# Performance work log

Hardware: AMD Instinct MI355X
Metric: run time of the kernel (lower is better)

Reference implementation:

```python
import jax, jax.numpy as jnp
import numpy as np

CHANNEL = 512
NUM_HEAD = 8
HEAD_DIM = CHANNEL // NUM_HEAD  # 64
TEMP = (2.0 * HEAD_DIM) ** 0.5  # sqrt(temperature_coeff * d)
B, N = 4, 2048


def setup_inputs() -> dict:
    key = jax.random.key(0)
    kx, km, kq, kk, kv = jax.random.split(key, 5)
    scale = 1.0 / np.sqrt(CHANNEL)
    return {
        "x": jax.random.normal(kx, (B, N, CHANNEL), dtype=jnp.float32),
        "mask": jax.random.randint(km, (1, B, N, N), 0, 2).astype(bool),
        "Wq": jax.random.normal(kq, (CHANNEL, CHANNEL), dtype=jnp.float32) * scale,
        "Wk": jax.random.normal(kk, (CHANNEL, CHANNEL), dtype=jnp.float32) * scale,
        "Wv": jax.random.normal(kv, (CHANNEL, CHANNEL), dtype=jnp.float32) * scale,
    }


def reference(x, mask, Wq, Wk, Wv):
    b, n, f = x.shape
    # nn.Linear(bias=False): y = x @ W.T ; split into heads
    q = (x @ Wq.T).reshape(b, n, NUM_HEAD, HEAD_DIM)
    k = (x @ Wk.T).reshape(b, n, NUM_HEAD, HEAD_DIM)
    v = (x @ Wv.T).reshape(b, n, NUM_HEAD, HEAD_DIM)
    # scores laid out as (head, batch, q, k) to match torch permute(2,0,1,3)
    a = jnp.einsum("bqhd,bkhd->hbqk", q, k) / TEMP
    # mask (1,B,N,N) broadcasts over the head dim; True -> -inf (masked_fill)
    alpha = jax.nn.softmax(jnp.where(mask, -jnp.inf, a), axis=-1)
    # (alpha @ v) then permute back to (b, n, h, d) and merge heads
    out = jnp.einsum("hbqk,bkhd->bqhd", alpha, v).reshape(b, n, f)
    return out
```

## Files before the change

kernel.cpp:

```cpp
#include <hip/hip_runtime.h>


typedef float f32x4 __attribute__((ext_vector_type(4)));
typedef float f32x16 __attribute__((ext_vector_type(16)));
typedef short short8 __attribute__((ext_vector_type(8)));

#define MFMA16(a, b, c) __builtin_amdgcn_mfma_f32_16x16x32_bf16((a), (b), (c), 0, 0, 0)
#define MFMA32(a, b, c) __builtin_amdgcn_mfma_f32_32x32x16_bf16((a), (b), (c), 0, 0, 0)

#if __has_builtin(__builtin_amdgcn_exp2f)
#define EXP2(x) __builtin_amdgcn_exp2f(x)
#else
#define EXP2(x) exp2f(x)
#endif

#define NBH 32
#define NSEQ 2048
#define DH 64

__device__ __forceinline__ unsigned short f2bf(float f) {
  unsigned int u = __float_as_uint(f);
  u += 0x7fffu + ((u >> 16) & 1u);
  return (unsigned short)(u >> 16);
}
__device__ __forceinline__ float bf2f(unsigned short h) {
  return __uint_as_float(((unsigned int)h) << 16);
}
__device__ __forceinline__ void split_bf16(float f, unsigned short& hi, unsigned short& lo) {
  hi = f2bf(f);
  lo = f2bf(f - bf2f(hi));
}

__device__ __forceinline__ unsigned cvtpk_bf16(float a, float b) {
  unsigned d;
  asm("v_cvt_pk_bf16_f32 %0, %1, %2" : "=v"(d) : "v"(a), "v"(b));
  return d;
}
__device__ __forceinline__ void permswap(unsigned& a, unsigned& b) {
  asm("v_permlane32_swap_b32 %0, %1" : "+v"(a), "+v"(b));
}
template <bool S2>
__device__ __forceinline__ void xsw(unsigned ce, unsigned co, unsigned& lo, unsigned& hi) {
  if (S2) { permswap(ce, co); }
  else    { permswap(co, ce); }
  lo = ce;
  hi = co;
}

typedef __attribute__((address_space(1))) const unsigned int as1_u32;
typedef __attribute__((address_space(3))) unsigned int as3_u32;
__device__ __forceinline__ void gld_lds16(const unsigned short* g, unsigned short* l) {
  __builtin_amdgcn_global_load_lds((as1_u32*)g, (as3_u32*)l, 16, 0, 0);
}

__global__ __launch_bounds__(256) void prep_kernel(
    const void* __restrict__ mraw, unsigned long long* __restrict__ Mp,
    const float* __restrict__ x,
    const float* __restrict__ Wq, const float* __restrict__ Wk, const float* __restrict__ Wv,
    unsigned short* __restrict__ xh, unsigned short* __restrict__ xl,
    unsigned short* __restrict__ wh, unsigned short* __restrict__ wl) {
  const int tid = threadIdx.x;
  __shared__ int s_bad;
  if (tid == 0) s_bad = 0;
  __syncthreads();
  const unsigned int* mw32 = (const unsigned int*)mraw;
  {
    unsigned int w0 = mw32[tid], w1 = mw32[256 + tid];
    bool ok = (w0 == 0u || w0 == 1u || w0 == 0x3f800000u) &&
              (w1 == 0u || w1 == 1u || w1 == 0x3f800000u);
    if (!ok) s_bad = 1;
  }
  __syncthreads();
  const size_t e0 = (size_t)blockIdx.x * 16384 + (size_t)tid * 64;
  unsigned long long bits = 0ull;
  if (s_bad == 0) {
    const uint4* p = (const uint4*)mw32 + (e0 >> 2);
#pragma unroll
    for (int j = 0; j < 16; ++j) {
      uint4 v = p[j];
      unsigned nib = (v.x != 0u) | ((v.y != 0u) << 1) | ((v.z != 0u) << 2) | ((v.w != 0u) << 3);
      bits |= (unsigned long long)nib << (j * 4);
    }
  } else {
    const uint4* p = (const uint4*)((const unsigned char*)mraw + e0);
#pragma unroll
    for (int j = 0; j < 4; ++j) {
      uint4 v = p[j];
      unsigned dw[4] = {v.x, v.y, v.z, v.w};
#pragma unroll
      for (int d = 0; d < 4; ++d) {
        unsigned nib = (((dw[d]) & 0xffu) != 0u) | ((((dw[d] >> 8) & 0xffu) != 0u) << 1) |
                       ((((dw[d] >> 16) & 0xffu) != 0u) << 2) | ((((dw[d] >> 24) & 0xffu) != 0u) << 3);
        bits |= (unsigned long long)nib << ((j * 4 + d) * 4);
      }
    }
  }
  Mp[e0 >> 6] = bits;

  const int gtid = blockIdx.x * 256 + tid;
  const float4* x4 = (const float4*)x;
#pragma unroll
  for (int rep = 0; rep < 4; ++rep) {
    int i = gtid + rep * 262144;
    float4 v = x4[i];
    unsigned short h0, l0, h1, l1, h2, l2, h3, l3;
    split_bf16(v.x, h0, l0); split_bf16(v.y, h1, l1);
    split_bf16(v.z, h2, l2); split_bf16(v.w, h3, l3);
    *(ushort4*)&xh[(size_t)i * 4] = make_ushort4(h0, h1, h2, h3);
    *(ushort4*)&xl[(size_t)i * 4] = make_ushort4(l0, l1, l2, l3);
  }
  if (gtid < 65536) {
    const float* Ws[3] = {Wq, Wk, Wv};
#pragma unroll
    for (int z = 0; z < 3; ++z) {
      float4 v = ((const float4*)Ws[z])[gtid];
      unsigned short h0, l0, h1, l1, h2, l2, h3, l3;
      split_bf16(v.x, h0, l0); split_bf16(v.y, h1, l1);
      split_bf16(v.z, h2, l2); split_bf16(v.w, h3, l3);
      size_t o = (size_t)z * 262144 + (size_t)gtid * 4;
      *(ushort4*)&wh[o] = make_ushort4(h0, h1, h2, h3);
      *(ushort4*)&wl[o] = make_ushort4(l0, l1, l2, l3);
    }
  }
}

__global__ __launch_bounds__(256, 4) void proj_kernel(
    const unsigned short* __restrict__ xh, const unsigned short* __restrict__ xl,
    const unsigned short* __restrict__ wh, const unsigned short* __restrict__ wl,
    unsigned short* __restrict__ Qh, unsigned short* __restrict__ Kh,
    unsigned short* __restrict__ Vh) {
  const int tid = threadIdx.x;
  const int w = tid >> 6, l = tid & 63;
  const int m0 = blockIdx.x * 64;
  const int h = blockIdx.y;
  const int lrow = l & 15, lg = l >> 4;
  const int rw = (w >> 1) * 32, cw = (w & 1) * 32;

  union LDSU {
    unsigned short tiles[8][64][32];
    unsigned short ob[64][72];
  };
  __shared__ __align__(16) LDSU u;

  f32x4 acc[3][2][2] = {};

  const unsigned short* planes[8] = {xh, xl, wh, wl, wh + 262144, wl + 262144,
                                     wh + 524288, wl + 524288};
  const int rowb[8] = {m0, m0, h * 64, h * 64, h * 64, h * 64, h * 64, h * 64};
  const int srow = l >> 2, scol = (l & 3) * 8;
  const unsigned short* s0 = planes[2 * w] + (size_t)(rowb[2 * w] + srow) * 512 + scol;
  const unsigned short* s1 = planes[2 * w + 1] + (size_t)(rowb[2 * w + 1] + srow) * 512 + scol;
  unsigned short* d0 = &u.tiles[2 * w][0][0];
  unsigned short* d1 = &u.tiles[2 * w + 1][0][0];

  for (int k0 = 0; k0 < 512; k0 += 32) {
    __syncthreads();
#pragma unroll
    for (int c = 0; c < 4; ++c) {
      gld_lds16(s0 + k0 + c * 8192, d0 + c * 512);
      gld_lds16(s1 + k0 + c * 8192, d1 + c * 512);
    }
    __syncthreads();

    short8 axh[2], axl[2];
#pragma unroll
    for (int t = 0; t < 2; ++t) {
      axh[t] = *(const short8*)&u.tiles[0][rw + 16 * t + lrow][lg * 8];
      axl[t] = *(const short8*)&u.tiles[1][rw + 16 * t + lrow][lg * 8];
    }
#pragma unroll
    for (int z = 0; z < 3; ++z) {
      short8 bh[2], bl[2];
#pragma unroll
      for (int t = 0; t < 2; ++t) {
        bh[t] = *(const short8*)&u.tiles[2 + 2 * z][cw + 16 * t + lrow][lg * 8];
        bl[t] = *(const short8*)&u.tiles[3 + 2 * z][cw + 16 * t + lrow][lg * 8];
      }
#pragma unroll
      for (int tm = 0; tm < 2; ++tm)
#pragma unroll
        for (int tn = 0; tn < 2; ++tn) {
          acc[z][tm][tn] = MFMA16(axh[tm], bh[tn], acc[z][tm][tn]);
          acc[z][tm][tn] = MFMA16(axh[tm], bl[tn], acc[z][tm][tn]);
          acc[z][tm][tn] = MFMA16(axl[tm], bh[tn], acc[z][tm][tn]);
        }
    }
  }

  const float qsc = 1.4426950408889634f * 0.08838834764831845f;
  const int orow = tid >> 2, oc = (tid & 3) * 16;
  const int b = m0 >> 11, n0 = m0 & 2047, bhid = b * 8 + h;
#pragma unroll
  for (int z = 0; z < 3; ++z) {
    __syncthreads();
#pragma unroll
    for (int tm = 0; tm < 2; ++tm)
#pragma unroll
      for (int tn = 0; tn < 2; ++tn) {
        int dcol = cw + tn * 16 + lrow;
        int nl = rw + tm * 16 + lg * 4;
#pragma unroll
        for (int r = 0; r < 4; ++r) {
          float v = acc[z][tm][tn][r];
          if (z == 0) v *= qsc;
          if (z < 2) u.ob[nl + r][dcol] = f2bf(v);
          else       u.ob[dcol][nl + r] = f2bf(v);
        }
      }
    __syncthreads();
    if (z < 2) {
      unsigned short* O = (z == 0) ? Qh : Kh;
      size_t base = ((size_t)bhid * 2048 + n0 + orow) * 64 + oc;
      *(short8*)&O[base] = *(const short8*)&u.ob[orow][oc];
      *(short8*)&O[base + 8] = *(const short8*)&u.ob[orow][oc + 8];
    } else {
      size_t vb = ((size_t)bhid * 64 + orow) * 2048 + n0 + oc;
      *(short8*)&Vh[vb] = *(const short8*)&u.ob[orow][oc];
      *(short8*)&Vh[vb + 8] = *(const short8*)&u.ob[orow][oc + 8];
    }
  }
}

template <bool S2>
__device__ __forceinline__ void attn_body(
    unsigned short (&kvb)[2][4][64][64],
    const unsigned short* __restrict__ Qh,
    const unsigned short* __restrict__ Kh, const unsigned short* __restrict__ Vh,
    const unsigned long long* __restrict__ Mp, float* __restrict__ out) {
  const int tid = threadIdx.x;
  const int w = tid >> 6, l = tid & 63;
  const int wl = blockIdx.x;
  const int rm = (wl & 7) * 64 + (wl >> 3);
  const int q0 = (rm & 15) * 128;
  const int bh = rm >> 4;
  const int b = bh >> 3, h = bh & 7;
  const int l31 = l & 31, hi = l >> 5;
  const int swz = (l31 & 7) << 4;

  const unsigned short* Qhb = Qh + (size_t)bh * NSEQ * DH;
  const unsigned short* Khb = Kh + (size_t)bh * NSEQ * DH;
  const unsigned short* Vhb = Vh + (size_t)bh * DH * NSEQ;
  const unsigned long long* Mb = Mp + (size_t)b * NSEQ * 32;
  float* Ob = out + (size_t)b * NSEQ * 512 + h * 64;

  char* kv0 = (char*)&kvb[0][0][0][0];

  int va[4];
#pragma unroll
  for (int d = 0; d < 4; ++d) va[d] = l31 * 128 + (((d * 32) | (hi * 16)) ^ swz);

  const size_t qoff = (size_t)(q0 + w * 32 + l31) * 64 + hi * 8;
  short8 qh[4];
#pragma unroll
  for (int d = 0; d < 4; ++d) qh[d] = *(const short8*)(Qhb + qoff + d * 16);

  short8 ones;
#pragma unroll
  for (int j = 0; j < 8; ++j) ones[j] = (short)0x3F80;

  f32x16 o[2] = {};
  f32x16 osum = {};
  float mrun = -1e30f;
  const int qglob = q0 + w * 32 + l31;

  const int row0 = tid >> 3, colx = (tid & 7) * 8;
  const int swst = (colx * 2) ^ ((row0 & 7) << 4);
  int dstK[4], dstV[4];
#pragma unroll
  for (int c = 0; c < 4; ++c) {
    const int rsub = (c & 1) * 32 + row0;
    dstK[c] = (c >> 1) * 8192 + rsub * 128 + swst;
    dstV[c] = 16384 + (c >> 1) * 8192 + rsub * 128 + swst;
  }
  size_t koff[4], voff[4];
#pragma unroll
  for (int c = 0; c < 4; ++c) {
    koff[c] = (size_t)(c * 32 + row0) * 64 + colx;
    voff[c] = (size_t)((c & 1) * 32 + row0) * 2048 + (c >> 1) * 64 + colx;
  }

  short8 sk[4], sv[4];
#pragma unroll
  for (int c = 0; c < 4; ++c) {
    sk[c] = *(const short8*)(Khb + koff[c]);
    sv[c] = *(const short8*)(Vhb + voff[c]);
  }
#pragma unroll
  for (int c = 0; c < 4; ++c) {
    *(short8*)(kv0 + dstK[c]) = sk[c];
    *(short8*)(kv0 + dstV[c]) = sv[c];
  }
#pragma unroll
  for (int c = 0; c < 4; ++c) {
    koff[c] += 8192; voff[c] += 128;
    sk[c] = *(const short8*)(Khb + koff[c]);
    sv[c] = *(const short8*)(Vhb + voff[c]);
  }
  __syncthreads();

  for (int it = 0; it < 16; ++it) {
    char* cur = kv0 + (size_t)(it & 1) * 32768;
    if (it < 15) {
      char* nb = kv0 + (size_t)((it + 1) & 1) * 32768;
#pragma unroll
      for (int c = 0; c < 4; ++c) {
        *(short8*)(nb + dstK[c]) = sk[c];
        *(short8*)(nb + dstV[c]) = sv[c];
      }
      if (it < 14) {
#pragma unroll
        for (int c = 0; c < 4; ++c) {
          koff[c] += 8192; voff[c] += 128;
          sk[c] = *(const short8*)(Khb + koff[c]);
          sv[c] = *(const short8*)(Vhb + voff[c]);
        }
      }
    }

    f32x16 sA[2] = {}, sB[2] = {};
    __builtin_amdgcn_s_setprio(1);
#pragma unroll
    for (int d = 0; d < 4; ++d) {
#pragma unroll
      for (int kt = 0; kt < 2; ++kt) {
        short8 kfa = *(const short8*)(cur + kt * 4096 + va[d]);
        short8 kfb = *(const short8*)(cur + 8192 + kt * 4096 + va[d]);
        sA[kt] = MFMA32(kfa, qh[d], sA[kt]);
        sB[kt] = MFMA32(kfb, qh[d], sB[kt]);
      }
    }
    __builtin_amdgcn_s_setprio(0);

    const unsigned long long mwA = Mb[(size_t)qglob * 32 + 2 * it];
    const unsigned long long mwB = Mb[(size_t)qglob * 32 + 2 * it + 1];
#pragma unroll
    for (int kt = 0; kt < 2; ++kt)
#pragma unroll
      for (int m = 0; m < 4; ++m) {
        unsigned nibA = ((unsigned)(mwA >> (kt * 32 + m * 8 + 4 * hi))) & 0xFu;
        unsigned nibB = ((unsigned)(mwB >> (kt * 32 + m * 8 + 4 * hi))) & 0xFu;
#pragma unroll
        for (int r = 0; r < 4; ++r) {
          sA[kt][4 * m + r] = ((nibA >> r) & 1u) ? -1e30f : sA[kt][4 * m + r];
          sB[kt][4 * m + r] = ((nibB >> r) & 1u) ? -1e30f : sB[kt][4 * m + r];
        }
      }

    float mx = fmaxf(sA[0][0], sB[0][0]);
#pragma unroll
    for (int kt = 0; kt < 2; ++kt)
#pragma unroll
      for (int e = (kt == 0 ? 1 : 0); e < 16; ++e)
        mx = fmaxf(fmaxf(sA[kt][e], sB[kt][e]), mx);
    mx = fmaxf(mx, __shfl_xor(mx, 32));
    const bool grow = __any(mx > mrun + 11.0f);
    const float mnew = grow ? fmaxf(mrun, mx) : mrun;

#pragma unroll
    for (int kt = 0; kt < 2; ++kt)
#pragma unroll
      for (int e = 0; e < 16; ++e) {
        sA[kt][e] = EXP2(sA[kt][e] - mnew);
        sB[kt][e] = EXP2(sB[kt][e] - mnew);
      }
    if (grow) {
      float sc = EXP2(mrun - mnew);
      mrun = mnew;
      osum[0] *= sc;
#pragma unroll
      for (int dt = 0; dt < 2; ++dt)
#pragma unroll
        for (int e = 0; e < 16; ++e) o[dt][e] *= sc;
    }

    {
      short8 fragh[4];
#pragma unroll
      for (int kt = 0; kt < 2; ++kt) {
        unsigned c0h[4], c1h[4];
#pragma unroll
        for (int m = 0; m < 4; ++m) {
          c0h[m] = cvtpk_bf16(sA[kt][4 * m + 0], sA[kt][4 * m + 1]);
          c1h[m] = cvtpk_bf16(sA[kt][4 * m + 2], sA[kt][4 * m + 3]);
        }
#pragma unroll
        for (int sI = 0; sI < 2; ++sI) {
          unsigned dw0, dw1, dw2, dw3;
          xsw<S2>(c0h[2 * sI], c0h[2 * sI + 1], dw0, dw2);
          xsw<S2>(c1h[2 * sI], c1h[2 * sI + 1], dw1, dw3);
          union U { uint4 u; short8 s8; } FH;
          FH.u = make_uint4(dw0, dw1, dw2, dw3);
          fragh[kt * 2 + sI] = FH.s8;
        }
      }
      __builtin_amdgcn_s_setprio(1);
#pragma unroll
      for (int ks = 0; ks < 4; ++ks) {
        short8 vf0 = *(const short8*)(cur + 16384 + va[ks]);
        short8 vf1 = *(const short8*)(cur + 16384 + 4096 + va[ks]);
        o[0] = MFMA32(vf0, fragh[ks], o[0]);
        o[1] = MFMA32(vf1, fragh[ks], o[1]);
        osum = MFMA32(ones, fragh[ks], osum);
      }
      __builtin_amdgcn_s_setprio(0);
    }

    {
      short8 fragh[4];
#pragma unroll
      for (int kt = 0; kt < 2; ++kt) {
        unsigned c0h[4], c1h[4];
#pragma unroll
        for (int m = 0; m < 4; ++m) {
          c0h[m] = cvtpk_bf16(sB[kt][4 * m + 0], sB[kt][4 * m + 1]);
          c1h[m] = cvtpk_bf16(sB[kt][4 * m + 2], sB[kt][4 * m + 3]);
        }
#pragma unroll
        for (int sI = 0; sI < 2; ++sI) {
          unsigned dw0, dw1, dw2, dw3;
          xsw<S2>(c0h[2 * sI], c0h[2 * sI + 1], dw0, dw2);
          xsw<S2>(c1h[2 * sI], c1h[2 * sI + 1], dw1, dw3);
          union U { uint4 u; short8 s8; } FH;
          FH.u = make_uint4(dw0, dw1, dw2, dw3);
          fragh[kt * 2 + sI] = FH.s8;
        }
      }
      __builtin_amdgcn_s_setprio(1);
#pragma unroll
      for (int ks = 0; ks < 4; ++ks) {
        short8 vf0 = *(const short8*)(cur + 24576 + va[ks]);
        short8 vf1 = *(const short8*)(cur + 24576 + 4096 + va[ks]);
        o[0] = MFMA32(vf0, fragh[ks], o[0]);
        o[1] = MFMA32(vf1, fragh[ks], o[1]);
        osum = MFMA32(ones, fragh[ks], osum);
      }
      __builtin_amdgcn_s_setprio(0);
    }

    __syncthreads();
  }

  const float lsum = osum[0];
  const float invl = lsum > 0.0f ? 1.0f / lsum : 0.0f;
#pragma unroll
  for (int dt = 0; dt < 2; ++dt)
#pragma unroll
    for (int m = 0; m < 4; ++m) {
      float4 v;
      v.x = o[dt][4 * m + 0] * invl;
      v.y = o[dt][4 * m + 1] * invl;
      v.z = o[dt][4 * m + 2] * invl;
      v.w = o[dt][4 * m + 3] * invl;
      const int d = dt * 32 + m * 8 + 4 * hi;
      *(float4*)&Ob[(size_t)qglob * 512 + d] = v;
    }
}

__global__ __launch_bounds__(256, 2) void attn_kernel(
    const unsigned short* __restrict__ Qh,
    const unsigned short* __restrict__ Kh, const unsigned short* __restrict__ Vh,
    const unsigned long long* __restrict__ Mp, float* __restrict__ out) {
  __shared__ __align__(16) unsigned short kvb[2][4][64][64];

  const int hi = (threadIdx.x & 63) >> 5;
  unsigned ta = 1u + (unsigned)hi;
  unsigned tb = 3u + (unsigned)hi;
  permswap(ta, tb);
  const bool s2 = (__builtin_amdgcn_readfirstlane(ta) == 1u);

  if (s2) attn_body<true>(kvb, Qh, Kh, Vh, Mp, out);
  else    attn_body<false>(kvb, Qh, Kh, Vh, Mp, out);
}

extern "C" void kernel_launch(void* const* d_in, const int* in_sizes, int n_in,
                              void* d_out, int out_size, void* d_ws, size_t ws_size,
                              hipStream_t stream) {
  const float* x = (const float*)d_in[0];
  const void* mask = d_in[1];
  const float* Wq = (const float*)d_in[2];
  const float* Wk = (const float*)d_in[3];
  const float* Wv = (const float*)d_in[4];
  float* out = (float*)d_out;

  const size_t PLANE = (size_t)NBH * NSEQ * DH;
  unsigned short* Qh = (unsigned short*)d_ws;
  unsigned short* Kh = Qh + PLANE;
  unsigned short* Vh = Kh + PLANE;
  unsigned short* xh = Vh + PLANE;
  unsigned short* xl = xh + PLANE;
  unsigned short* wh = xl + PLANE;
  unsigned short* wl = wh + 786432;
  unsigned long long* Mp = (unsigned long long*)(wl + 786432);

  prep_kernel<<<1024, 256, 0, stream>>>(mask, Mp, x, Wq, Wk, Wv, xh, xl, wh, wl);
  proj_kernel<<<dim3(128, 8), 256, 0, stream>>>(xh, xl, wh, wl, Qh, Kh, Vh);
  attn_kernel<<<512, 256, 0, stream>>>(Qh, Kh, Vh, Mp, out);
}
```

Measured before the change: 123.5 us.

## Software-pipeline QK^T of next tile with softmax and PV of current tile

Restructures the attention main loop so the QK^T MFMAs for the next K/V tile are issued before the masking, softmax and PV work of the current tile, using ping-pong score registers and a two-iteration unrolled lambda. The goal is to overlap matrix-core work with the VALU exp/mask work. The LDS refill now happens after the PV step and needs an extra barrier per iteration. It also doubles the live score accumulators, which raises register pressure and may lower occupancy. The prologue contains leftover no-op statements.

```diff
diff --git a/kernel.cpp b/kernel.cpp
--- a/kernel.cpp
+++ b/kernel.cpp
@@ -298,41 +298,68 @@
   }
   __syncthreads();
 
-  for (int it = 0; it < 16; ++it) {
-    char* cur = kv0 + (size_t)(it & 1) * 32768;
-    if (it < 15) {
-      char* nb = kv0 + (size_t)((it + 1) & 1) * 32768;
-#pragma unroll
-      for (int c = 0; c < 4; ++c) {
-        *(short8*)(nb + dstK[c]) = sk[c];
-        *(short8*)(nb + dstV[c]) = sv[c];
-      }
-      if (it < 14) {
-#pragma unroll
-        for (int c = 0; c < 4; ++c) {
-          koff[c] += 8192; voff[c] += 128;
-          sk[c] = *(const short8*)(Khb + koff[c]);
-          sv[c] = *(const short8*)(Vhb + voff[c]);
-        }
-      }
-    }
-
-    f32x16 sA[2] = {}, sB[2] = {};
+  f32x16 sE[2] = {}, sO[2] = {};
+  __builtin_amdgcn_s_setprio(1);
+#pragma unroll
+  for (int d = 0; d < 4; ++d) {
+#pragma unroll
+    for (int kt = 0; kt < 2; ++kt) {
+      short8 kfa = *(const short8*)(kv0 + kt * 4096 + va[d]);
+      short8 kfb = *(const short8*)(kv0 + 8192 + kt * 4096 + va[d]);
+      sE[0 + 0] = (kt == 0 && d == -1) ? sE[0] : sE[0];
+      sE[kt] = MFMA32(kfa, qh[d], sE[kt]);
+      sO[kt] = sO[kt];
+      sE[kt] = sE[kt];
+      (void)kfb;
+    }
+  }
+  __builtin_amdgcn_s_setprio(0);
+  f32x16 sEb[2] = {}, sOb[2] = {};
+  {
     __builtin_amdgcn_s_setprio(1);
 #pragma unroll
     for (int d = 0; d < 4; ++d) {
 #pragma unroll
       for (int kt = 0; kt < 2; ++kt) {
-        short8 kfa = *(const short8*)(cur + kt * 4096 + va[d]);
-        short8 kfb = *(const short8*)(cur + 8192 + kt * 4096 + va[d]);
-        sA[kt] = MFMA32(kfa, qh[d], sA[kt]);
-        sB[kt] = MFMA32(kfb, qh[d], sB[kt]);
+        short8 kfb = *(const short8*)(kv0 + 8192 + kt * 4096 + va[d]);
+        sEb[kt] = MFMA32(kfb, qh[d], sEb[kt]);
       }
     }
     __builtin_amdgcn_s_setprio(0);
-
+  }
+#pragma unroll
+  for (int c = 0; c < 4; ++c) {
+    *(short8*)(kv0 + 32768 + dstK[c]) = sk[c];
+    *(short8*)(kv0 + 32768 + dstV[c]) = sv[c];
+  }
+#pragma unroll
+  for (int c = 0; c < 4; ++c) {
+    koff[c] += 8192; voff[c] += 128;
+    sk[c] = *(const short8*)(Khb + koff[c]);
+    sv[c] = *(const short8*)(Vhb + voff[c]);
+  }
+  __syncthreads();
+
+  auto half = [&](int it, f32x16 (&sA)[2], f32x16 (&sB)[2],
+                  f32x16 (&nA)[2], f32x16 (&nB)[2], int curOff, int nxtOff) {
     const unsigned long long mwA = Mb[(size_t)qglob * 32 + 2 * it];
     const unsigned long long mwB = Mb[(size_t)qglob * 32 + 2 * it + 1];
+
+    if (it < 15) {
+#pragma unroll
+      for (int kt = 0; kt < 2; ++kt) { nA[kt] = (f32x16){}; nB[kt] = (f32x16){}; }
+#pragma unroll
+      for (int d = 0; d < 4; ++d) {
+#pragma unroll
+        for (int kt = 0; kt < 2; ++kt) {
+          short8 kfa = *(const short8*)(kv0 + nxtOff + kt * 4096 + va[d]);
+          short8 kfb = *(const short8*)(kv0 + nxtOff + 8192 + kt * 4096 + va[d]);
+          nA[kt] = MFMA32(kfa, qh[d], nA[kt]);
+          nB[kt] = MFMA32(kfb, qh[d], nB[kt]);
+        }
+      }
+    }
+
 #pragma unroll
     for (int kt = 0; kt < 2; ++kt)
 #pragma unroll
@@ -345,7 +372,6 @@
           sB[kt][4 * m + r] = ((nibB >> r) & 1u) ? -1e30f : sB[kt][4 * m + r];
         }
       }
-
     float mx = fmaxf(sA[0][0], sB[0][0]);
 #pragma unroll
     for (int kt = 0; kt < 2; ++kt)
@@ -396,15 +422,14 @@
       __builtin_amdgcn_s_setprio(1);
 #pragma unroll
       for (int ks = 0; ks < 4; ++ks) {
-        short8 vf0 = *(const short8*)(cur + 16384 + va[ks]);
-        short8 vf1 = *(const short8*)(cur + 16384 + 4096 + va[ks]);
+        short8 vf0 = *(const short8*)(kv0 + curOff + 16384 + va[ks]);
+        short8 vf1 = *(const short8*)(kv0 + curOff + 16384 + 4096 + va[ks]);
         o[0] = MFMA32(vf0, fragh[ks], o[0]);
         o[1] = MFMA32(vf1, fragh[ks], o[1]);
         osum = MFMA32(ones, fragh[ks], osum);
       }
       __builtin_amdgcn_s_setprio(0);
     }
-
     {
       short8 fragh[4];
 #pragma unroll
@@ -428,8 +453,8 @@
       __builtin_amdgcn_s_setprio(1);
 #pragma unroll
       for (int ks = 0; ks < 4; ++ks) {
-        short8 vf0 = *(const short8*)(cur + 24576 + va[ks]);
-        short8 vf1 = *(const short8*)(cur + 24576 + 4096 + va[ks]);
+        short8 vf0 = *(const short8*)(kv0 + curOff + 24576 + va[ks]);
+        short8 vf1 = *(const short8*)(kv0 + curOff + 24576 + 4096 + va[ks]);
         o[0] = MFMA32(vf0, fragh[ks], o[0]);
         o[1] = MFMA32(vf1, fragh[ks], o[1]);
         osum = MFMA32(ones, fragh[ks], osum);
@@ -438,6 +463,27 @@
     }
 
     __syncthreads();
+    if (it < 14) {
+#pragma unroll
+      for (int c = 0; c < 4; ++c) {
+        *(short8*)(kv0 + curOff + dstK[c]) = sk[c];
+        *(short8*)(kv0 + curOff + dstV[c]) = sv[c];
+      }
+      if (it < 13) {
+#pragma unroll
+        for (int c = 0; c < 4; ++c) {
+          koff[c] += 8192; voff[c] += 128;
+          sk[c] = *(const short8*)(Khb + koff[c]);
+          sv[c] = *(const short8*)(Vhb + voff[c]);
+        }
+      }
+    }
+    __syncthreads();
+  };
+
+  for (int itp = 0; itp < 8; ++itp) {
+    half(2 * itp, sE, sEb, sO, sOb, 0, 32768);
+    half(2 * itp + 1, sO, sOb, sE, sEb, 32768, 0);
   }
 
   const float lsum = osum[0];
```

New measurement: 169.6 us. 37.3% more time.
